# Kernel tuning notes

Measured on AMD Instinct MI355X. Metric: run time of the kernel, lower is better.

Reference implementation:

```python
import jax, jax.numpy as jnp
import numpy as np
import math

L, DIN, DZ, H, C, NQ, NP = 768, 384, 128, 12, 16, 4, 6
C_SQU = 1.0 / math.sqrt(C)            # scalar qk scale
W_C = math.sqrt(2.0 / (9 * NQ))       # point-distance scale


def _w(key, fan_in, fan_out):
    return jax.random.normal(key, (fan_in, fan_out), dtype=jnp.float32) / math.sqrt(fan_in)


def setup_inputs() -> dict:
    key = jax.random.key(0)
    ks = jax.random.split(key, 20)
    inp = {
        "s": jax.random.normal(ks[0], (L, DIN), dtype=jnp.float32),
        "z": jax.random.normal(ks[1], (L, L, DZ), dtype=jnp.float32),
        "rot": jax.random.normal(ks[2], (L, 3, 3), dtype=jnp.float32),
        "trans": jax.random.normal(ks[3], (L, 3), dtype=jnp.float32),
        "Wq1": _w(ks[4], DIN, H * C),
        "Wk1": _w(ks[5], DIN, H * C),
        "Wv1": _w(ks[6], DIN, H * C),
        "Wq2": _w(ks[7], DIN, H * NQ * 3),
        "Wk2": _w(ks[8], DIN, H * NQ * 3),
        "Wv3": _w(ks[9], DIN, H * NP * 3),
        "Wz": _w(ks[10], DZ, H),
        "W1": _w(ks[11], H * DZ, DIN),
        "b1": jnp.zeros((DIN,), dtype=jnp.float32),
        "W2": _w(ks[12], H * C, DIN),
        "b2": jnp.zeros((DIN,), dtype=jnp.float32),
        "W3": _w(ks[13], H * NP * 3, DIN),
        "b3": jnp.zeros((DIN,), dtype=jnp.float32),
        "gamma": jnp.zeros((H,), dtype=jnp.float32),
    }
    return inp


def ipa_transform(x, rot, trans):
    # x: [L,H,P,3] local points -> global: rot @ x + trans
    return jnp.einsum('lij,lhpj->lhpi', rot, x) + trans[:, None, None, :]


def ipa_inverse_transform(x, rot, trans):
    # global -> local: rot^T @ (x - trans)
    return jnp.einsum('lji,lhpj->lhpi', rot, x - trans[:, None, None, :])


def reference(s, z, rot, trans, Wq1, Wk1, Wv1, Wq2, Wk2, Wv3, Wz,
              W1, b1, W2, b2, W3, b3, gamma):
    q1 = (s @ Wq1).reshape(L, H, C)
    k1 = (s @ Wk1).reshape(L, H, C)
    v1 = (s @ Wv1).reshape(L, H, C)
    att = jnp.einsum('ihc,jhc->ijh', q1, k1) * C_SQU          # [L,L,H]
    bias_z = z @ Wz                                           # [L,L,H]
    q2 = ipa_transform((s @ Wq2).reshape(L, H, NQ, 3), rot, trans)
    k2 = ipa_transform((s @ Wk2).reshape(L, H, NQ, 3), rot, trans)
    # squared-distance map sum over query points & xyz, via |q|^2+|k|^2-2qk
    sq = jnp.sum(q2 * q2, axis=(-2, -1))                      # [L,H]
    sk = jnp.sum(k2 * k2, axis=(-2, -1))                      # [L,H]
    cross = jnp.einsum('ihqt,jhqt->ijh', q2, k2)              # [L,L,H]
    dismap = sq[:, None, :] + sk[None, :, :] - 2.0 * cross
    # NOTE: no softmax in the original module — raw scores weight the values.
    att = att + bias_z - jax.nn.softplus(gamma)[None, None, :] * dismap * (W_C * 0.5)
    o1 = jnp.einsum('ijh,ijd->ihd', att, z)                   # [L,H,DZ]
    o2 = jnp.einsum('jhc,ijh->ihc', v1, att)                  # [L,H,C]
    v3 = ipa_transform((s @ Wv3).reshape(L, H, NP, 3), rot, trans)
    o3 = ipa_inverse_transform(jnp.einsum('jhpt,ijh->ihpt', v3, att), rot, trans)
    out = (o1.reshape(L, -1) @ W1 + b1) \
        + (o2.reshape(L, -1) @ W2 + b2) \
        + (o3.reshape(L, -1) @ W3 + b3)
    return out
```

## Files before the change

### kernel.cpp

```cpp
#include <hip/hip_runtime.h>
#include <math.h>
#include <stdint.h>

#define LL 768
#define DIN 384
#define HH 12
#define NLIN 1080
#define WC_HALF 0.11785113019775792f
#define C_SQU 0.25f

#define OFF_LIN    0u
#define OFF_V1P    829440u
#define OFF_V3P    903168u
#define OFF_QBH    986112u
#define OFF_QBL    1133568u
#define OFF_KBH    1281024u
#define OFF_KBL    1428480u
#define OFF_WZ     1575936u
#define OFF_SQWH   1576960u
#define OFF_SKWH   1586176u
#define OFF_SX     1595392u
#define OFF_O1     8673280u
#define OFF_O2     9852928u
#define OFF_O3     10000384u

typedef __attribute__((ext_vector_type(8))) short short8v;
typedef __attribute__((ext_vector_type(4))) float float4v;

__device__ __forceinline__ ushort f2bu(float f) {
    union { float f; uint32_t u; } v; v.f = f;
    uint32_t r = (v.u + 0x7FFFu + ((v.u >> 16) & 1u)) >> 16;
    return (ushort)r;
}
__device__ __forceinline__ float bu2f(ushort u) {
    union { uint32_t u; float f; } v; v.u = ((uint32_t)u) << 16; return v.f;
}
__device__ __forceinline__ float blo2f(uint32_t u) {
    union { uint32_t u; float f; } v; v.u = u << 16; return v.f;
}
__device__ __forceinline__ float bhi2f(uint32_t u) {
    union { uint32_t u; float f; } v; v.u = u & 0xFFFF0000u; return v.f;
}
__device__ __forceinline__ int fswz(int j) {
    return (((j >> 3) << 1) | ((j >> 1) & 1)) << 4;
}

__global__ __launch_bounds__(256) void gemm_lin_kernel(
    const float* __restrict__ s,
    const float* __restrict__ Wq1, const float* __restrict__ Wk1,
    const float* __restrict__ Wv1, const float* __restrict__ Wq2,
    const float* __restrict__ Wk2, const float* __restrict__ Wv3,
    float* __restrict__ lin)
{
    const int n0 = blockIdx.x * 64;
    const int i0 = blockIdx.y * 64;
    const int tid = threadIdx.x;
    __shared__ float sT[64][17];
    __shared__ float wT[16][65];
    const int tc = tid & 15, tr = tid >> 4;
    float acc[4][4] = {};
    for (int k0 = 0; k0 < DIN; k0 += 16) {
        __syncthreads();
        for (int idx = tid; idx < 1024; idx += 256) {
            int r = idx >> 4, kk = idx & 15;
            sT[r][kk] = s[(size_t)(i0 + r) * DIN + k0 + kk];
        }
        for (int idx = tid; idx < 1024; idx += 256) {
            int kk = idx >> 6, c = idx & 63;
            int col = n0 + c;
            float v = 0.f;
            if (col < NLIN) {
                const float* W; int nout, cc2;
                if      (col < 192) { W = Wq1; nout = 192; cc2 = col; }
                else if (col < 384) { W = Wk1; nout = 192; cc2 = col - 192; }
                else if (col < 576) { W = Wv1; nout = 192; cc2 = col - 384; }
                else if (col < 720) { W = Wq2; nout = 144; cc2 = col - 576; }
                else if (col < 864) { W = Wk2; nout = 144; cc2 = col - 720; }
                else                { W = Wv3; nout = 216; cc2 = col - 864; }
                v = W[(size_t)(k0 + kk) * nout + cc2];
            }
            wT[kk][c] = v;
        }
        __syncthreads();
        #pragma unroll
        for (int kk = 0; kk < 16; ++kk) {
            float a[4], b[4];
            #pragma unroll
            for (int r = 0; r < 4; ++r) a[r] = sT[tr * 4 + r][kk];
            #pragma unroll
            for (int c = 0; c < 4; ++c) b[c] = wT[kk][tc * 4 + c];
            #pragma unroll
            for (int r = 0; r < 4; ++r)
                #pragma unroll
                for (int c = 0; c < 4; ++c) acc[r][c] += a[r] * b[c];
        }
    }
    for (int r = 0; r < 4; ++r)
        for (int c = 0; c < 4; ++c) {
            int col = n0 + tc * 4 + c;
            if (col < NLIN)
                lin[(size_t)(i0 + tr * 4 + r) * NLIN + col] = acc[r][c];
        }
}

__global__ __launch_bounds__(192) void transform_kernel(
    const float* __restrict__ lin, const float* __restrict__ rot,
    const float* __restrict__ trans, const float* __restrict__ gamma,
    const float* __restrict__ Wz,
    ushort* __restrict__ v1q, ushort* __restrict__ v3q,
    ushort* __restrict__ qbh, ushort* __restrict__ qbl,
    ushort* __restrict__ kbh, ushort* __restrict__ kbl,
    ushort* __restrict__ wzpack,
    float* __restrict__ sqwh, float* __restrict__ skwh)
{
    const int l = blockIdx.x;
    const int tid = threadIdx.x;
    __shared__ float q2s[144], k2s[144], sqp[48], skp[48];
    __shared__ float v3s[216];
    __shared__ float whs[12];
    __shared__ float R[9], T[3];
    if (tid < 9) R[tid] = rot[l * 9 + tid];
    if (tid >= 9 && tid < 12) T[tid - 9] = trans[l * 3 + tid - 9];
    __syncthreads();
    if (tid < 48) {
        const float* x = &lin[(size_t)l * NLIN + 576 + tid * 3];
        float x0 = x[0], x1 = x[1], x2 = x[2], ss = 0.f;
        #pragma unroll
        for (int i2 = 0; i2 < 3; ++i2) {
            float v = R[i2*3+0]*x0 + R[i2*3+1]*x1 + R[i2*3+2]*x2 + T[i2];
            q2s[tid * 3 + i2] = v; ss += v * v;
        }
        sqp[tid] = ss;
    } else if (tid < 96) {
        int t2 = tid - 48;
        const float* x = &lin[(size_t)l * NLIN + 720 + t2 * 3];
        float x0 = x[0], x1 = x[1], x2 = x[2], ss = 0.f;
        #pragma unroll
        for (int i2 = 0; i2 < 3; ++i2) {
            float v = R[i2*3+0]*x0 + R[i2*3+1]*x1 + R[i2*3+2]*x2 + T[i2];
            k2s[t2 * 3 + i2] = v; ss += v * v;
        }
        skp[t2] = ss;
    } else if (tid < 168) {
        int t2 = tid - 96;
        const float* x = &lin[(size_t)l * NLIN + 864 + t2 * 3];
        float x0 = x[0], x1 = x[1], x2 = x[2];
        #pragma unroll
        for (int i2 = 0; i2 < 3; ++i2) {
            float v = R[i2*3+0]*x0 + R[i2*3+1]*x1 + R[i2*3+2]*x2 + T[i2];
            v3s[t2 * 3 + i2] = v;
        }
    }
    __syncthreads();
    if (tid < 12) {
        float sq = sqp[tid*4] + sqp[tid*4+1] + sqp[tid*4+2] + sqp[tid*4+3];
        float sk = skp[tid*4] + skp[tid*4+1] + skp[tid*4+2] + skp[tid*4+3];
        float w = logf(1.0f + expf(gamma[tid])) * WC_HALF;
        whs[tid] = w;
        sqwh[tid * 768 + l] = w * sq;
        skwh[tid * 768 + l] = w * sk;
    }
    __syncthreads();
    const int tt = l >> 5, jj = l & 31;
    if (tid < 192)
        v1q[((size_t)tt * 192 + tid) * 32 + jj] =
            f2bu(lin[(size_t)l * NLIN + 384 + tid]);
    for (int c = tid; c < 216; c += 192)
        v3q[((size_t)tt * 216 + c) * 32 + jj] = f2bu(v3s[c]);
    for (int idx = tid; idx < 384; idx += 192) {
        int h = idx >> 5, k = idx & 31;
        float qv, kv;
        if (k < 16) {
            qv = lin[(size_t)l * NLIN + h * 16 + k];
            kv = C_SQU * lin[(size_t)l * NLIN + 192 + h * 16 + k];
        } else if (k < 28) {
            int u = k - 16;
            qv = q2s[h * 12 + u];
            kv = 2.0f * whs[h] * k2s[h * 12 + u];
        } else { qv = 0.0f; kv = 0.0f; }
        size_t base = ((size_t)h * 768 + l) * 32 + k;
        ushort qh = f2bu(qv), kh = f2bu(kv);
        qbh[base] = qh; qbl[base] = f2bu(qv - bu2f(qh));
        kbh[base] = kh; kbl[base] = f2bu(kv - bu2f(kh));
    }
    if (l == 0) {
        for (int idx = tid; idx < 2048; idx += 192) {
            int kb = idx >> 9, lane = (idx >> 3) & 63, e = idx & 7;
            int d = kb * 32 + (lane >> 4) * 8 + e, h = lane & 15;
            wzpack[idx] = (h < 12) ? f2bu(Wz[d * 12 + h]) : (ushort)0;
        }
    }
}

__global__ __launch_bounds__(256) void sextra_kernel(
    const ushort* __restrict__ qbh, const ushort* __restrict__ qbl,
    const ushort* __restrict__ kbh, const ushort* __restrict__ kbl,
    const float* __restrict__ sqwh, const float* __restrict__ skwh,
    float* __restrict__ sx)
{
    const int tid = threadIdx.x;
    const int wv = tid >> 6, lane = tid & 63, lm = lane & 15, g = lane >> 4;
    const int i0 = blockIdx.x * 16;
    const int jb = blockIdx.y * 64 + wv * 16;
    #pragma unroll 4
    for (int h = 0; h < 12; ++h) {
        size_t qoff = ((size_t)h * 768 + i0 + lm) * 32 + g * 8;
        size_t koff = ((size_t)h * 768 + jb + lm) * 32 + g * 8;
        short8v ah = *(const short8v*)(qbh + qoff);
        short8v al = *(const short8v*)(qbl + qoff);
        short8v bh = *(const short8v*)(kbh + koff);
        short8v bl = *(const short8v*)(kbl + koff);
        float4v c1 = {0.f, 0.f, 0.f, 0.f};
        float4v c2 = {0.f, 0.f, 0.f, 0.f};
        c1 = __builtin_amdgcn_mfma_f32_16x16x32_bf16(ah, bh, c1, 0, 0, 0);
        c2 = __builtin_amdgcn_mfma_f32_16x16x32_bf16(ah, bl, c2, 0, 0, 0);
        c2 = __builtin_amdgcn_mfma_f32_16x16x32_bf16(al, bh, c2, 0, 0, 0);
        float skv = skwh[h * 768 + jb + lm];
        #pragma unroll
        for (int r = 0; r < 4; ++r) {
            int ii = i0 + g * 4 + r;
            sx[((size_t)ii * 12 + h) * 768 + jb + lm] =
                (c1[r] + c2[r]) - sqwh[h * 768 + ii] - skv;
        }
    }
}

__global__ __launch_bounds__(256) void attn_kernel(
    const float* __restrict__ z, const ushort* __restrict__ v1q,
    const ushort* __restrict__ v3q, const float* __restrict__ sx,
    const ushort* __restrict__ wzp,
    const float* __restrict__ rot, const float* __restrict__ trans,
    float* __restrict__ o1, float* __restrict__ o2, float* __restrict__ o3l)
{
    const int i = blockIdx.x, tid = threadIdx.x;
    const int wv = tid >> 6, lane = tid & 63, lm = lane & 15, g = lane >> 4;
    __shared__ __attribute__((aligned(16))) char zrow[2][32 * 256];
    __shared__ __attribute__((aligned(16))) char attbh[16 * 80];
    __shared__ __attribute__((aligned(16))) char attbl[16 * 80];
    __shared__ __attribute__((aligned(16))) float attf[16][36];
    __shared__ float o3s[216];

    short8v wzf[4];
    #pragma unroll
    for (int kb = 0; kb < 4; ++kb)
        wzf[kb] = *(const short8v*)(wzp + (kb * 64 + lane) * 8);

    const float4* zsrc = (const float4*)(z + (size_t)i * (LL * 128));
    const int jA = wv * 16 + lm;
    const int h2 = tid >> 4;
    const int h3 = tid / 18;

    {
        float4 z0[4];
        #pragma unroll
        for (int s = 0; s < 4; ++s) z0[s] = zsrc[s * 256 + tid];
        #pragma unroll
        for (int s = 0; s < 4; ++s) {
            int k4 = s * 256 + tid, j = k4 >> 5, d0 = (k4 & 31) * 4;
            float4 v = z0[s];
            ushort b0 = f2bu(v.x), b1 = f2bu(v.y), b2 = f2bu(v.z), b3 = f2bu(v.w);
            uint32_t lo = b0 | ((uint32_t)b1 << 16), hi = b2 | ((uint32_t)b3 << 16);
            *(uint64_t*)(&zrow[0][j * 256 + ((d0 * 2) ^ fswz(j))]) =
                (uint64_t)lo | ((uint64_t)hi << 32);
        }
    }
    float sxr[4] = {0.f, 0.f, 0.f, 0.f};
    if (wv < 2 && g < 3) {
        #pragma unroll
        for (int r = 0; r < 4; ++r)
            sxr[r] = sx[((size_t)i * 12 + g * 4 + r) * 768 + jA];
    }
    __syncthreads();

    float4v acc1[2] = {{0.f,0.f,0.f,0.f}, {0.f,0.f,0.f,0.f}};
    float acc2 = 0.f, acc3 = 0.f;
    int p = 0;

    for (int t = 0; t < 24; ++t) {
        const int j0 = t * 32;
        float4 zreg[4];
        if (t < 23) {
            #pragma unroll
            for (int s = 0; s < 4; ++s)
                zreg[s] = zsrc[(size_t)(t + 1) * 1024 + s * 256 + tid];
        }
        uint4 v1x[4], v3x[4];
        if (tid < 192) {
            const uint4* pv = (const uint4*)(v1q + ((size_t)t * 192 + tid) * 32);
            #pragma unroll
            for (int c4 = 0; c4 < 4; ++c4) v1x[c4] = pv[c4];
        }
        if (tid < 216) {
            const uint4* pv = (const uint4*)(v3q + ((size_t)t * 216 + tid) * 32);
            #pragma unroll
            for (int c4 = 0; c4 < 4; ++c4) v3x[c4] = pv[c4];
        }
        float sxn[4] = {0.f, 0.f, 0.f, 0.f};
        if (wv < 2 && g < 3 && t < 23) {
            #pragma unroll
            for (int r = 0; r < 4; ++r)
                sxn[r] = sx[((size_t)i * 12 + g * 4 + r) * 768 + j0 + 32 + jA];
        }
        if (wv < 2) {
            float4v bias = {0.f, 0.f, 0.f, 0.f};
            #pragma unroll
            for (int kb = 0; kb < 4; ++kb) {
                short8v bz = *(const short8v*)(
                    &zrow[p][jA * 256 + ((kb * 64 + g * 16) ^ fswz(jA))]);
                bias = __builtin_amdgcn_mfma_f32_16x16x32_bf16(wzf[kb], bz, bias, 0, 0, 0);
            }
            #pragma unroll
            for (int r = 0; r < 4; ++r) {
                int h = g * 4 + r;
                float att = bias[r] + sxr[r];
                attf[h][jA] = att;
                ushort hi = f2bu(att);
                *(ushort*)(&attbh[h * 80 + jA * 2]) = hi;
                *(ushort*)(&attbl[h * 80 + jA * 2]) = f2bu(att - bu2f(hi));
            }
        }
        __syncthreads();
        {
            short8v ah = *(const short8v*)(&attbh[lm * 80 + g * 16]);
            short8v al = *(const short8v*)(&attbl[lm * 80 + g * 16]);
            #pragma unroll
            for (int q = 0; q < 2; ++q) {
                const int b = wv * 2 + q;
                short8v bf;
                #pragma unroll
                for (int e = 0; e < 8; ++e) {
                    int jj = g * 8 + e;
                    bf[e] = *(const short*)(&zrow[p][jj * 256 +
                              (((b * 16 + lm) * 2) ^ fswz(jj))]);
                }
                acc1[q] = __builtin_amdgcn_mfma_f32_16x16x32_bf16(ah, bf, acc1[q], 0, 0, 0);
                acc1[q] = __builtin_amdgcn_mfma_f32_16x16x32_bf16(al, bf, acc1[q], 0, 0, 0);
            }
        }
        if (tid < 192) {
            const float4* af = (const float4*)(&attf[h2][0]);
            #pragma unroll
            for (int c4 = 0; c4 < 4; ++c4) {
                float4 a0 = af[2 * c4], a1 = af[2 * c4 + 1];
                uint4 w = v1x[c4];
                acc2 += a0.x * blo2f(w.x) + a0.y * bhi2f(w.x)
                      + a0.z * blo2f(w.y) + a0.w * bhi2f(w.y)
                      + a1.x * blo2f(w.z) + a1.y * bhi2f(w.z)
                      + a1.z * blo2f(w.w) + a1.w * bhi2f(w.w);
            }
        }
        if (tid < 216) {
            const float4* af = (const float4*)(&attf[h3][0]);
            #pragma unroll
            for (int c4 = 0; c4 < 4; ++c4) {
                float4 a0 = af[2 * c4], a1 = af[2 * c4 + 1];
                uint4 w = v3x[c4];
                acc3 += a0.x * blo2f(w.x) + a0.y * bhi2f(w.x)
                      + a0.z * blo2f(w.y) + a0.w * bhi2f(w.y)
                      + a1.x * blo2f(w.z) + a1.y * bhi2f(w.z)
                      + a1.z * blo2f(w.w) + a1.w * bhi2f(w.w);
            }
        }
        if (t < 23) {
            #pragma unroll
            for (int s = 0; s < 4; ++s) {
                int k4 = s * 256 + tid, j = k4 >> 5, d0 = (k4 & 31) * 4;
                float4 v = zreg[s];
                ushort b0 = f2bu(v.x), b1 = f2bu(v.y), b2 = f2bu(v.z), b3 = f2bu(v.w);
                uint32_t lo = b0 | ((uint32_t)b1 << 16), hi = b2 | ((uint32_t)b3 << 16);
                *(uint64_t*)(&zrow[p ^ 1][j * 256 + ((d0 * 2) ^ fswz(j))]) =
                    (uint64_t)lo | ((uint64_t)hi << 32);
            }
        }
        __syncthreads();
        #pragma unroll
        for (int r = 0; r < 4; ++r) sxr[r] = sxn[r];
        p ^= 1;
    }
    if (g < 3) {
        #pragma unroll
        for (int q = 0; q < 2; ++q) {
            const int b = wv * 2 + q;
            #pragma unroll
            for (int r = 0; r < 4; ++r)
                o1[(size_t)i * 1536 + (g * 4 + r) * 128 + b * 16 + lm] = acc1[q][r];
        }
    }
    if (tid < 192) o2[(size_t)i * 192 + tid] = acc2;
    if (tid < 216) o3s[tid] = acc3;
    __syncthreads();
    if (tid < 72) {
        float x0 = o3s[tid * 3 + 0] - trans[i * 3 + 0];
        float x1 = o3s[tid * 3 + 1] - trans[i * 3 + 1];
        float x2 = o3s[tid * 3 + 2] - trans[i * 3 + 2];
        const float* R = &rot[(size_t)i * 9];
        o3l[(size_t)i * 216 + tid * 3 + 0] = R[0]*x0 + R[3]*x1 + R[6]*x2;
        o3l[(size_t)i * 216 + tid * 3 + 1] = R[1]*x0 + R[4]*x1 + R[7]*x2;
        o3l[(size_t)i * 216 + tid * 3 + 2] = R[2]*x0 + R[5]*x1 + R[8]*x2;
    }
}

#define KCH 324
__global__ __launch_bounds__(384) void proj_kernel(
    const float* __restrict__ o1, const float* __restrict__ o2,
    const float* __restrict__ o3l,
    const float* __restrict__ W1, const float* __restrict__ W2,
    const float* __restrict__ W3,
    float* __restrict__ part)
{
    const int it = blockIdx.x, kt = blockIdx.y;
    const int tid = threadIdx.x;
    const int kbeg = kt * KCH, kend = kbeg + KCH;
    __shared__ float olds[16][KCH];
    for (int idx = tid; idx < 16 * KCH; idx += 384) {
        int r = idx / KCH, kk = idx % KCH;
        int k = kbeg + kk;
        int i = it * 16 + r;
        float v;
        if (k < 1536)      v = o1[(size_t)i * 1536 + k];
        else if (k < 1728) v = o2[(size_t)i * 192 + k - 1536];
        else               v = o3l[(size_t)i * 216 + k - 1728];
        olds[r][kk] = v;
    }
    __syncthreads();
    float acc[16] = {};
    {
        int s0 = kbeg, s1 = (kend < 1536) ? kend : 1536;
        for (int k = s0; k < s1; ++k) {
            float w = W1[(size_t)k * 384 + tid];
            int kk = k - kbeg;
            #pragma unroll
            for (int r = 0; r < 16; ++r) acc[r] += olds[r][kk] * w;
        }
    }
    {
        int s0 = (kbeg > 1536) ? kbeg : 1536, s1 = (kend < 1728) ? kend : 1728;
        for (int k = s0; k < s1; ++k) {
            float w = W2[(size_t)(k - 1536) * 384 + tid];
            int kk = k - kbeg;
            #pragma unroll
            for (int r = 0; r < 16; ++r) acc[r] += olds[r][kk] * w;
        }
    }
    {
        int s0 = (kbeg > 1728) ? kbeg : 1728, s1 = kend;
        for (int k = s0; k < s1; ++k) {
            float w = W3[(size_t)(k - 1728) * 384 + tid];
            int kk = k - kbeg;
            #pragma unroll
            for (int r = 0; r < 16; ++r) acc[r] += olds[r][kk] * w;
        }
    }
    for (int r = 0; r < 16; ++r)
        part[((size_t)kt * LL + it * 16 + r) * 384 + tid] = acc[r];
}

__global__ __launch_bounds__(256) void final_kernel(
    const float* __restrict__ part,
    const float* __restrict__ b1, const float* __restrict__ b2,
    const float* __restrict__ b3, float* __restrict__ out)
{
    int idx = blockIdx.x * 256 + threadIdx.x;
    if (idx < LL * 384) {
        int n = idx % 384;
        float v = b1[n] + b2[n] + b3[n];
        #pragma unroll
        for (int kt = 0; kt < 6; ++kt) v += part[(size_t)kt * 294912 + idx];
        out[idx] = v;
    }
}

extern "C" void kernel_launch(void* const* d_in, const int* in_sizes, int n_in,
                              void* d_out, int out_size, void* d_ws, size_t ws_size,
                              hipStream_t stream) {
    const float* s     = (const float*)d_in[0];
    const float* z     = (const float*)d_in[1];
    const float* rot   = (const float*)d_in[2];
    const float* trans = (const float*)d_in[3];
    const float* Wq1   = (const float*)d_in[4];
    const float* Wk1   = (const float*)d_in[5];
    const float* Wv1   = (const float*)d_in[6];
    const float* Wq2   = (const float*)d_in[7];
    const float* Wk2   = (const float*)d_in[8];
    const float* Wv3   = (const float*)d_in[9];
    const float* Wz    = (const float*)d_in[10];
    const float* W1    = (const float*)d_in[11];
    const float* b1    = (const float*)d_in[12];
    const float* W2    = (const float*)d_in[13];
    const float* b2    = (const float*)d_in[14];
    const float* W3    = (const float*)d_in[15];
    const float* b3    = (const float*)d_in[16];
    const float* gamma = (const float*)d_in[17];
    float* ws  = (float*)d_ws;
    float* out = (float*)d_out;

    float*  lin  = ws + OFF_LIN;
    ushort* v1q  = (ushort*)(ws + OFF_V1P);
    ushort* v3q  = (ushort*)(ws + OFF_V3P);
    ushort* qbh  = (ushort*)(ws + OFF_QBH);
    ushort* qbl  = (ushort*)(ws + OFF_QBL);
    ushort* kbh  = (ushort*)(ws + OFF_KBH);
    ushort* kbl  = (ushort*)(ws + OFF_KBL);
    ushort* wzp  = (ushort*)(ws + OFF_WZ);
    float*  sqwh = ws + OFF_SQWH;
    float*  skwh = ws + OFF_SKWH;
    float*  sx   = ws + OFF_SX;
    float*  o1   = ws + OFF_O1;
    float*  o2   = ws + OFF_O2;
    float*  o3l  = ws + OFF_O3;
    float*  part = ws + OFF_SX;

    dim3 gA(17, 12);
    gemm_lin_kernel<<<gA, 256, 0, stream>>>(s, Wq1, Wk1, Wv1, Wq2, Wk2, Wv3, lin);
    transform_kernel<<<LL, 192, 0, stream>>>(lin, rot, trans, gamma, Wz,
                                             v1q, v3q, qbh, qbl, kbh, kbl, wzp,
                                             sqwh, skwh);
    dim3 gS(48, 12);
    sextra_kernel<<<gS, 256, 0, stream>>>(qbh, qbl, kbh, kbl, sqwh, skwh, sx);
    attn_kernel<<<LL, 256, 0, stream>>>(z, v1q, v3q, sx, wzp, rot, trans,
                                        o1, o2, o3l);
    dim3 gC(48, 6);
    proj_kernel<<<gC, 384, 0, stream>>>(o1, o2, o3l, W1, W2, W3, part);
    final_kernel<<<(LL * 384 + 255) / 256, 256, 0, stream>>>(part, b1, b2, b3, out);
}
```

Before: 333.2 us.

## Split attention j-range across two blocks per row with separate reduction kernel

Each attention row is now processed by two blocks, each covering half of the key range (12 of 24 tiles). Partial o1/o2/o3 sums go to new workspace buffers, and a new reduce kernel adds them and applies the inverse frame transform. This doubles the grid to 1536 blocks, so the 768-block launch fills the GPU's compute units more evenly. The cost is an extra kernel launch, partial-sum write and read traffic, and a shorter per-block pipeline.

Measured after the change: 325.0 us. 1.03x faster.

```diff
diff --git a/kernel.cpp b/kernel.cpp
--- a/kernel.cpp
+++ b/kernel.cpp
@@ -23,6 +23,9 @@
 #define OFF_O1     8673280u
 #define OFF_O2     9852928u
 #define OFF_O3     10000384u
+#define OFF_PO1    10166272u
+#define OFF_PO2    12525568u
+#define OFF_PO3    12820480u
 
 typedef __attribute__((ext_vector_type(8))) short short8v;
 typedef __attribute__((ext_vector_type(4))) float float4v;
@@ -229,16 +232,16 @@
     const float* __restrict__ z, const ushort* __restrict__ v1q,
     const ushort* __restrict__ v3q, const float* __restrict__ sx,
     const ushort* __restrict__ wzp,
-    const float* __restrict__ rot, const float* __restrict__ trans,
-    float* __restrict__ o1, float* __restrict__ o2, float* __restrict__ o3l)
-{
-    const int i = blockIdx.x, tid = threadIdx.x;
+    float* __restrict__ po1, float* __restrict__ po2, float* __restrict__ po3)
+{
+    const int bid = blockIdx.x, tid = threadIdx.x;
+    const int i = bid >> 1, half = bid & 1;
+    const int t0 = half * 12;
     const int wv = tid >> 6, lane = tid & 63, lm = lane & 15, g = lane >> 4;
     __shared__ __attribute__((aligned(16))) char zrow[2][32 * 256];
     __shared__ __attribute__((aligned(16))) char attbh[16 * 80];
     __shared__ __attribute__((aligned(16))) char attbl[16 * 80];
     __shared__ __attribute__((aligned(16))) float attf[16][36];
-    __shared__ float o3s[216];
 
     short8v wzf[4];
     #pragma unroll
@@ -253,7 +256,7 @@
     {
         float4 z0[4];
         #pragma unroll
-        for (int s = 0; s < 4; ++s) z0[s] = zsrc[s * 256 + tid];
+        for (int s = 0; s < 4; ++s) z0[s] = zsrc[(size_t)t0 * 1024 + s * 256 + tid];
         #pragma unroll
         for (int s = 0; s < 4; ++s) {
             int k4 = s * 256 + tid, j = k4 >> 5, d0 = (k4 & 31) * 4;
@@ -268,7 +271,7 @@
     if (wv < 2 && g < 3) {
         #pragma unroll
         for (int r = 0; r < 4; ++r)
-            sxr[r] = sx[((size_t)i * 12 + g * 4 + r) * 768 + jA];
+            sxr[r] = sx[((size_t)i * 12 + g * 4 + r) * 768 + t0 * 32 + jA];
     }
     __syncthreads();
 
@@ -276,27 +279,28 @@
     float acc2 = 0.f, acc3 = 0.f;
     int p = 0;
 
-    for (int t = 0; t < 24; ++t) {
-        const int j0 = t * 32;
+    for (int t = 0; t < 12; ++t) {
+        const int tt = t0 + t;
+        const int j0 = tt * 32;
         float4 zreg[4];
-        if (t < 23) {
+        if (t < 11) {
             #pragma unroll
             for (int s = 0; s < 4; ++s)
-                zreg[s] = zsrc[(size_t)(t + 1) * 1024 + s * 256 + tid];
+                zreg[s] = zsrc[(size_t)(tt + 1) * 1024 + s * 256 + tid];
         }
         uint4 v1x[4], v3x[4];
         if (tid < 192) {
-            const uint4* pv = (const uint4*)(v1q + ((size_t)t * 192 + tid) * 32);
+            const uint4* pv = (const uint4*)(v1q + ((size_t)tt * 192 + tid) * 32);
             #pragma unroll
             for (int c4 = 0; c4 < 4; ++c4) v1x[c4] = pv[c4];
         }
         if (tid < 216) {
-            const uint4* pv = (const uint4*)(v3q + ((size_t)t * 216 + tid) * 32);
+            const uint4* pv = (const uint4*)(v3q + ((size_t)tt * 216 + tid) * 32);
             #pragma unroll
             for (int c4 = 0; c4 < 4; ++c4) v3x[c4] = pv[c4];
         }
         float sxn[4] = {0.f, 0.f, 0.f, 0.f};
-        if (wv < 2 && g < 3 && t < 23) {
+        if (wv < 2 && g < 3 && t < 11) {
             #pragma unroll
             for (int r = 0; r < 4; ++r)
                 sxn[r] = sx[((size_t)i * 12 + g * 4 + r) * 768 + j0 + 32 + jA];
@@ -361,7 +365,7 @@
                       + a1.z * blo2f(w.w) + a1.w * bhi2f(w.w);
             }
         }
-        if (t < 23) {
+        if (t < 11) {
             #pragma unroll
             for (int s = 0; s < 4; ++s) {
                 int k4 = s * 256 + tid, j = k4 >> 5, d0 = (k4 & 31) * 4;
@@ -383,11 +387,30 @@
             const int b = wv * 2 + q;
             #pragma unroll
             for (int r = 0; r < 4; ++r)
-                o1[(size_t)i * 1536 + (g * 4 + r) * 128 + b * 16 + lm] = acc1[q][r];
-        }
-    }
-    if (tid < 192) o2[(size_t)i * 192 + tid] = acc2;
-    if (tid < 216) o3s[tid] = acc3;
+                po1[(size_t)bid * 1536 + (g * 4 + r) * 128 + b * 16 + lm] = acc1[q][r];
+        }
+    }
+    if (tid < 192) po2[(size_t)bid * 192 + tid] = acc2;
+    if (tid < 216) po3[(size_t)bid * 216 + tid] = acc3;
+}
+
+__global__ __launch_bounds__(256) void reduce_kernel(
+    const float* __restrict__ po1, const float* __restrict__ po2,
+    const float* __restrict__ po3,
+    const float* __restrict__ rot, const float* __restrict__ trans,
+    float* __restrict__ o1, float* __restrict__ o2, float* __restrict__ o3l)
+{
+    const int i = blockIdx.x, tid = threadIdx.x;
+    __shared__ float o3s[216];
+    const size_t a1 = (size_t)(2 * i) * 1536, b1 = (size_t)(2 * i + 1) * 1536;
+    for (int c = tid; c < 1536; c += 256)
+        o1[(size_t)i * 1536 + c] = po1[a1 + c] + po1[b1 + c];
+    if (tid < 192)
+        o2[(size_t)i * 192 + tid] = po2[(size_t)(2 * i) * 192 + tid]
+                                  + po2[(size_t)(2 * i + 1) * 192 + tid];
+    if (tid < 216)
+        o3s[tid] = po3[(size_t)(2 * i) * 216 + tid]
+                 + po3[(size_t)(2 * i + 1) * 216 + tid];
     __syncthreads();
     if (tid < 72) {
         float x0 = o3s[tid * 3 + 0] - trans[i * 3 + 0];
@@ -508,6 +531,9 @@
     float*  o1   = ws + OFF_O1;
     float*  o2   = ws + OFF_O2;
     float*  o3l  = ws + OFF_O3;
+    float*  po1  = ws + OFF_PO1;
+    float*  po2  = ws + OFF_PO2;
+    float*  po3  = ws + OFF_PO3;
     float*  part = ws + OFF_SX;
 
     dim3 gA(17, 12);
@@ -517,8 +543,8 @@
                                              sqwh, skwh);
     dim3 gS(48, 12);
     sextra_kernel<<<gS, 256, 0, stream>>>(qbh, qbl, kbh, kbl, sqwh, skwh, sx);
-    attn_kernel<<<LL, 256, 0, stream>>>(z, v1q, v3q, sx, wzp, rot, trans,
-                                        o1, o2, o3l);
+    attn_kernel<<<LL * 2, 256, 0, stream>>>(z, v1q, v3q, sx, wzp, po1, po2, po3);
+    reduce_kernel<<<LL, 256, 0, stream>>>(po1, po2, po3, rot, trans, o1, o2, o3l);
     dim3 gC(48, 6);
     proj_kernel<<<gC, 384, 0, stream>>>(o1, o2, o3l, W1, W2, W3, part);
     final_kernel<<<(LL * 384 + 255) / 256, 256, 0, stream>>>(part, b1, b2, b3, out);
```

## Split attention over j-halves, move value products to MFMA kernel, fuse final reduction

Applied to the files above, without the earlier changes.

The attention kernel now splits each row's j range across two blocks and only computes the z-weighted output, writing full attention scores back into the sx buffer. A new ov_kernel computes the v1 and v3 weighted sums per head with bf16 hi/lo MFMAs over a transposed value layout, then applies the inverse frame transform. sextra gets one block per head, and the projection kernel loops over all K chunks itself, summing the two partial o1 halves and adding biases so the final reduction kernel goes away. This trades scalar per-thread value dot products and the attention kernel's serial j loop for more parallelism and tensor-core use, at the cost of an extra read and write of the attention matrix and fewer blocks in the projection.

Result: slower. 702.6 us (+110.9%).

```diff
diff --git a/kernel.cpp b/kernel.cpp
--- a/kernel.cpp
+++ b/kernel.cpp
@@ -10,19 +10,18 @@
 #define C_SQU 0.25f
 
 #define OFF_LIN    0u
-#define OFF_V1P    829440u
-#define OFF_V3P    903168u
-#define OFF_QBH    986112u
-#define OFF_QBL    1133568u
-#define OFF_KBH    1281024u
-#define OFF_KBL    1428480u
-#define OFF_WZ     1575936u
-#define OFF_SQWH   1576960u
-#define OFF_SKWH   1586176u
-#define OFF_SX     1595392u
-#define OFF_O1     8673280u
-#define OFF_O2     9852928u
-#define OFF_O3     10000384u
+#define OFF_VT     829440u
+#define OFF_QBH    1050624u
+#define OFF_QBL    1198080u
+#define OFF_KBH    1345536u
+#define OFF_KBL    1492992u
+#define OFF_WZ     1640448u
+#define OFF_SQWH   1641472u
+#define OFF_SKWH   1650688u
+#define OFF_SX     1659904u
+#define OFF_O2     8737792u
+#define OFF_O3     8885248u
+#define OFF_PO1    9051136u
 
 typedef __attribute__((ext_vector_type(8))) short short8v;
 typedef __attribute__((ext_vector_type(4))) float float4v;
@@ -34,12 +33,6 @@
 }
 __device__ __forceinline__ float bu2f(ushort u) {
     union { uint32_t u; float f; } v; v.u = ((uint32_t)u) << 16; return v.f;
-}
-__device__ __forceinline__ float blo2f(uint32_t u) {
-    union { uint32_t u; float f; } v; v.u = u << 16; return v.f;
-}
-__device__ __forceinline__ float bhi2f(uint32_t u) {
-    union { uint32_t u; float f; } v; v.u = u & 0xFFFF0000u; return v.f;
 }
 __device__ __forceinline__ int fswz(int j) {
     return (((j >> 3) << 1) | ((j >> 1) & 1)) << 4;
@@ -107,7 +100,7 @@
     const float* __restrict__ lin, const float* __restrict__ rot,
     const float* __restrict__ trans, const float* __restrict__ gamma,
     const float* __restrict__ Wz,
-    ushort* __restrict__ v1q, ushort* __restrict__ v3q,
+    ushort* __restrict__ vT,
     ushort* __restrict__ qbh, ushort* __restrict__ qbl,
     ushort* __restrict__ kbh, ushort* __restrict__ kbl,
     ushort* __restrict__ wzpack,
@@ -161,12 +154,12 @@
         skwh[tid * 768 + l] = w * sk;
     }
     __syncthreads();
-    const int tt = l >> 5, jj = l & 31;
-    if (tid < 192)
-        v1q[((size_t)tt * 192 + tid) * 32 + jj] =
-            f2bu(lin[(size_t)l * NLIN + 384 + tid]);
-    for (int c = tid; c < 216; c += 192)
-        v3q[((size_t)tt * 216 + c) * 32 + jj] = f2bu(v3s[c]);
+    for (int w = tid; w < 408; w += 192) {
+        int h = w / 34, c = w % 34;
+        float v = (c < 16) ? lin[(size_t)l * NLIN + 384 + h * 16 + c]
+                           : v3s[h * 18 + (c - 16)];
+        vT[((size_t)h * 48 + c) * 768 + l] = f2bu(v);
+    }
     for (int idx = tid; idx < 384; idx += 192) {
         int h = idx >> 5, k = idx & 31;
         float qv, kv;
@@ -202,43 +195,38 @@
     const int wv = tid >> 6, lane = tid & 63, lm = lane & 15, g = lane >> 4;
     const int i0 = blockIdx.x * 16;
     const int jb = blockIdx.y * 64 + wv * 16;
-    #pragma unroll 4
-    for (int h = 0; h < 12; ++h) {
-        size_t qoff = ((size_t)h * 768 + i0 + lm) * 32 + g * 8;
-        size_t koff = ((size_t)h * 768 + jb + lm) * 32 + g * 8;
-        short8v ah = *(const short8v*)(qbh + qoff);
-        short8v al = *(const short8v*)(qbl + qoff);
-        short8v bh = *(const short8v*)(kbh + koff);
-        short8v bl = *(const short8v*)(kbl + koff);
-        float4v c1 = {0.f, 0.f, 0.f, 0.f};
-        float4v c2 = {0.f, 0.f, 0.f, 0.f};
-        c1 = __builtin_amdgcn_mfma_f32_16x16x32_bf16(ah, bh, c1, 0, 0, 0);
-        c2 = __builtin_amdgcn_mfma_f32_16x16x32_bf16(ah, bl, c2, 0, 0, 0);
-        c2 = __builtin_amdgcn_mfma_f32_16x16x32_bf16(al, bh, c2, 0, 0, 0);
-        float skv = skwh[h * 768 + jb + lm];
-        #pragma unroll
-        for (int r = 0; r < 4; ++r) {
-            int ii = i0 + g * 4 + r;
-            sx[((size_t)ii * 12 + h) * 768 + jb + lm] =
-                (c1[r] + c2[r]) - sqwh[h * 768 + ii] - skv;
-        }
+    const int h = blockIdx.z;
+    size_t qoff = ((size_t)h * 768 + i0 + lm) * 32 + g * 8;
+    size_t koff = ((size_t)h * 768 + jb + lm) * 32 + g * 8;
+    short8v ah = *(const short8v*)(qbh + qoff);
+    short8v al = *(const short8v*)(qbl + qoff);
+    short8v bh = *(const short8v*)(kbh + koff);
+    short8v bl = *(const short8v*)(kbl + koff);
+    float4v c1 = {0.f, 0.f, 0.f, 0.f};
+    float4v c2 = {0.f, 0.f, 0.f, 0.f};
+    c1 = __builtin_amdgcn_mfma_f32_16x16x32_bf16(ah, bh, c1, 0, 0, 0);
+    c2 = __builtin_amdgcn_mfma_f32_16x16x32_bf16(ah, bl, c2, 0, 0, 0);
+    c2 = __builtin_amdgcn_mfma_f32_16x16x32_bf16(al, bh, c2, 0, 0, 0);
+    float skv = skwh[h * 768 + jb + lm];
+    #pragma unroll
+    for (int r = 0; r < 4; ++r) {
+        int ii = i0 + g * 4 + r;
+        sx[((size_t)ii * 12 + h) * 768 + jb + lm] =
+            (c1[r] + c2[r]) - sqwh[h * 768 + ii] - skv;
     }
 }
 
 __global__ __launch_bounds__(256) void attn_kernel(
-    const float* __restrict__ z, const ushort* __restrict__ v1q,
-    const ushort* __restrict__ v3q, const float* __restrict__ sx,
-    const ushort* __restrict__ wzp,
-    const float* __restrict__ rot, const float* __restrict__ trans,
-    float* __restrict__ o1, float* __restrict__ o2, float* __restrict__ o3l)
+    const float* __restrict__ z, const ushort* __restrict__ wzp,
+    float* sxa,
+    float* __restrict__ po1)
 {
-    const int i = blockIdx.x, tid = threadIdx.x;
+    const int bid = blockIdx.x, tid = threadIdx.x;
+    const int i = bid >> 1, t0 = (bid & 1) * 12;
     const int wv = tid >> 6, lane = tid & 63, lm = lane & 15, g = lane >> 4;
     __shared__ __attribute__((aligned(16))) char zrow[2][32 * 256];
     __shared__ __attribute__((aligned(16))) char attbh[16 * 80];
     __shared__ __attribute__((aligned(16))) char attbl[16 * 80];
-    __shared__ __attribute__((aligned(16))) float attf[16][36];
-    __shared__ float o3s[216];
 
     short8v wzf[4];
     #pragma unroll
@@ -247,13 +235,11 @@
 
     const float4* zsrc = (const float4*)(z + (size_t)i * (LL * 128));
     const int jA = wv * 16 + lm;
-    const int h2 = tid >> 4;
-    const int h3 = tid / 18;
 
     {
         float4 z0[4];
         #pragma unroll
-        for (int s = 0; s < 4; ++s) z0[s] = zsrc[s * 256 + tid];
+        for (int s = 0; s < 4; ++s) z0[s] = zsrc[(size_t)t0 * 1024 + s * 256 + tid];
         #pragma unroll
         for (int s = 0; s < 4; ++s) {
             int k4 = s * 256 + tid, j = k4 >> 5, d0 = (k4 & 31) * 4;
@@ -268,38 +254,26 @@
     if (wv < 2 && g < 3) {
         #pragma unroll
         for (int r = 0; r < 4; ++r)
-            sxr[r] = sx[((size_t)i * 12 + g * 4 + r) * 768 + jA];
+            sxr[r] = sxa[((size_t)i * 12 + g * 4 + r) * 768 + t0 * 32 + jA];
     }
     __syncthreads();
 
     float4v acc1[2] = {{0.f,0.f,0.f,0.f}, {0.f,0.f,0.f,0.f}};
-    float acc2 = 0.f, acc3 = 0.f;
     int p = 0;
 
-    for (int t = 0; t < 24; ++t) {
-        const int j0 = t * 32;
+    for (int t = 0; t < 12; ++t) {
+        const int tt = t0 + t, j0 = tt * 32;
         float4 zreg[4];
-        if (t < 23) {
+        if (t < 11) {
             #pragma unroll
             for (int s = 0; s < 4; ++s)
-                zreg[s] = zsrc[(size_t)(t + 1) * 1024 + s * 256 + tid];
-        }
-        uint4 v1x[4], v3x[4];
-        if (tid < 192) {
-            const uint4* pv = (const uint4*)(v1q + ((size_t)t * 192 + tid) * 32);
-            #pragma unroll
-            for (int c4 = 0; c4 < 4; ++c4) v1x[c4] = pv[c4];
-        }
-        if (tid < 216) {
-            const uint4* pv = (const uint4*)(v3q + ((size_t)t * 216 + tid) * 32);
-            #pragma unroll
-            for (int c4 = 0; c4 < 4; ++c4) v3x[c4] = pv[c4];
+                zreg[s] = zsrc[(size_t)(tt + 1) * 1024 + s * 256 + tid];
         }
         float sxn[4] = {0.f, 0.f, 0.f, 0.f};
-        if (wv < 2 && g < 3 && t < 23) {
+        if (wv < 2 && g < 3 && t < 11) {
             #pragma unroll
             for (int r = 0; r < 4; ++r)
-                sxn[r] = sx[((size_t)i * 12 + g * 4 + r) * 768 + j0 + 32 + jA];
+                sxn[r] = sxa[((size_t)i * 12 + g * 4 + r) * 768 + j0 + 32 + jA];
         }
         if (wv < 2) {
             float4v bias = {0.f, 0.f, 0.f, 0.f};
@@ -313,10 +287,11 @@
             for (int r = 0; r < 4; ++r) {
                 int h = g * 4 + r;
                 float att = bias[r] + sxr[r];
-                attf[h][jA] = att;
                 ushort hi = f2bu(att);
                 *(ushort*)(&attbh[h * 80 + jA * 2]) = hi;
                 *(ushort*)(&attbl[h * 80 + jA * 2]) = f2bu(att - bu2f(hi));
+                if (g < 3)
+                    sxa[((size_t)i * 12 + h) * 768 + j0 + jA] = att;
             }
         }
         __syncthreads();
@@ -337,31 +312,7 @@
                 acc1[q] = __builtin_amdgcn_mfma_f32_16x16x32_bf16(al, bf, acc1[q], 0, 0, 0);
             }
         }
-        if (tid < 192) {
-            const float4* af = (const float4*)(&attf[h2][0]);
-            #pragma unroll
-            for (int c4 = 0; c4 < 4; ++c4) {
-                float4 a0 = af[2 * c4], a1 = af[2 * c4 + 1];
-                uint4 w = v1x[c4];
-                acc2 += a0.x * blo2f(w.x) + a0.y * bhi2f(w.x)
-                      + a0.z * blo2f(w.y) + a0.w * bhi2f(w.y)
-                      + a1.x * blo2f(w.z) + a1.y * bhi2f(w.z)
-                      + a1.z * blo2f(w.w) + a1.w * bhi2f(w.w);
-            }
-        }
-        if (tid < 216) {
-            const float4* af = (const float4*)(&attf[h3][0]);
-            #pragma unroll
-            for (int c4 = 0; c4 < 4; ++c4) {
-                float4 a0 = af[2 * c4], a1 = af[2 * c4 + 1];
-                uint4 w = v3x[c4];
-                acc3 += a0.x * blo2f(w.x) + a0.y * bhi2f(w.x)
-                      + a0.z * blo2f(w.y) + a0.w * bhi2f(w.y)
-                      + a1.x * blo2f(w.z) + a1.y * bhi2f(w.z)
-                      + a1.z * blo2f(w.w) + a1.w * bhi2f(w.w);
-            }
-        }
-        if (t < 23) {
+        if (t < 11) {
             #pragma unroll
             for (int s = 0; s < 4; ++s) {
                 int k4 = s * 256 + tid, j = k4 >> 5, d0 = (k4 & 31) * 4;
@@ -383,91 +334,133 @@
             const int b = wv * 2 + q;
             #pragma unroll
             for (int r = 0; r < 4; ++r)
-                o1[(size_t)i * 1536 + (g * 4 + r) * 128 + b * 16 + lm] = acc1[q][r];
-        }
-    }
-    if (tid < 192) o2[(size_t)i * 192 + tid] = acc2;
-    if (tid < 216) o3s[tid] = acc3;
+                po1[(size_t)bid * 1536 + (g * 4 + r) * 128 + b * 16 + lm] = acc1[q][r];
+        }
+    }
+}
+
+__global__ __launch_bounds__(64) void ov_kernel(
+    const float* __restrict__ att, const ushort* __restrict__ vT,
+    const float* __restrict__ rot, const float* __restrict__ trans,
+    float* __restrict__ o2, float* __restrict__ o3l)
+{
+    const int i0 = blockIdx.x * 16;
+    const int h = blockIdx.y;
+    const int lane = threadIdx.x;
+    const int lm = lane & 15, g = lane >> 4;
+    __shared__ float o3s[16][18];
+
+    float4v acc0 = {0.f,0.f,0.f,0.f};
+    float4v acc1 = {0.f,0.f,0.f,0.f};
+    float4v acc2 = {0.f,0.f,0.f,0.f};
+    const float* arow = att + ((size_t)(i0 + lm) * 12 + h) * 768;
+    const ushort* vbase = vT + (size_t)h * 48 * 768;
+    for (int kt = 0; kt < 24; ++kt) {
+        const float4* ap = (const float4*)(arow + kt * 32 + g * 8);
+        float4 a0 = ap[0], a1 = ap[1];
+        float av[8] = {a0.x, a0.y, a0.z, a0.w, a1.x, a1.y, a1.z, a1.w};
+        short8v ah, al;
+        #pragma unroll
+        for (int e = 0; e < 8; ++e) {
+            ushort hi = f2bu(av[e]);
+            ah[e] = (short)hi;
+            al[e] = (short)f2bu(av[e] - bu2f(hi));
+        }
+        const int kq = kt * 32 + g * 8;
+        short8v b0 = *(const short8v*)(vbase + (size_t)(0 * 16 + lm) * 768 + kq);
+        short8v b1 = *(const short8v*)(vbase + (size_t)(1 * 16 + lm) * 768 + kq);
+        short8v b2 = *(const short8v*)(vbase + (size_t)(2 * 16 + lm) * 768 + kq);
+        acc0 = __builtin_amdgcn_mfma_f32_16x16x32_bf16(ah, b0, acc0, 0, 0, 0);
+        acc0 = __builtin_amdgcn_mfma_f32_16x16x32_bf16(al, b0, acc0, 0, 0, 0);
+        acc1 = __builtin_amdgcn_mfma_f32_16x16x32_bf16(ah, b1, acc1, 0, 0, 0);
+        acc1 = __builtin_amdgcn_mfma_f32_16x16x32_bf16(al, b1, acc1, 0, 0, 0);
+        acc2 = __builtin_amdgcn_mfma_f32_16x16x32_bf16(ah, b2, acc2, 0, 0, 0);
+        acc2 = __builtin_amdgcn_mfma_f32_16x16x32_bf16(al, b2, acc2, 0, 0, 0);
+    }
+    #pragma unroll
+    for (int r = 0; r < 4; ++r)
+        o2[(size_t)(i0 + g * 4 + r) * 192 + h * 16 + lm] = acc0[r];
+    #pragma unroll
+    for (int r = 0; r < 4; ++r) {
+        int row = g * 4 + r;
+        o3s[row][lm < 16 ? lm : 0] = acc1[r];
+        if (lm < 2) o3s[row][16 + lm] = acc2[r];
+    }
     __syncthreads();
-    if (tid < 72) {
-        float x0 = o3s[tid * 3 + 0] - trans[i * 3 + 0];
-        float x1 = o3s[tid * 3 + 1] - trans[i * 3 + 1];
-        float x2 = o3s[tid * 3 + 2] - trans[i * 3 + 2];
-        const float* R = &rot[(size_t)i * 9];
-        o3l[(size_t)i * 216 + tid * 3 + 0] = R[0]*x0 + R[3]*x1 + R[6]*x2;
-        o3l[(size_t)i * 216 + tid * 3 + 1] = R[1]*x0 + R[4]*x1 + R[7]*x2;
-        o3l[(size_t)i * 216 + tid * 3 + 2] = R[2]*x0 + R[5]*x1 + R[8]*x2;
+    for (int it = lane; it < 96; it += 64) {
+        int row = it / 6, pp = it % 6;
+        int ii = i0 + row;
+        const float* R = &rot[(size_t)ii * 9];
+        float x0 = o3s[row][pp * 3 + 0] - trans[ii * 3 + 0];
+        float x1 = o3s[row][pp * 3 + 1] - trans[ii * 3 + 1];
+        float x2 = o3s[row][pp * 3 + 2] - trans[ii * 3 + 2];
+        o3l[(size_t)ii * 216 + h * 18 + pp * 3 + 0] = R[0]*x0 + R[3]*x1 + R[6]*x2;
+        o3l[(size_t)ii * 216 + h * 18 + pp * 3 + 1] = R[1]*x0 + R[4]*x1 + R[7]*x2;
+        o3l[(size_t)ii * 216 + h * 18 + pp * 3 + 2] = R[2]*x0 + R[5]*x1 + R[8]*x2;
     }
 }
 
 #define KCH 324
 __global__ __launch_bounds__(384) void proj_kernel(
-    const float* __restrict__ o1, const float* __restrict__ o2,
+    const float* __restrict__ po1, const float* __restrict__ o2,
     const float* __restrict__ o3l,
     const float* __restrict__ W1, const float* __restrict__ W2,
     const float* __restrict__ W3,
-    float* __restrict__ part)
-{
-    const int it = blockIdx.x, kt = blockIdx.y;
-    const int tid = threadIdx.x;
-    const int kbeg = kt * KCH, kend = kbeg + KCH;
-    __shared__ float olds[16][KCH];
-    for (int idx = tid; idx < 16 * KCH; idx += 384) {
-        int r = idx / KCH, kk = idx % KCH;
-        int k = kbeg + kk;
-        int i = it * 16 + r;
-        float v;
-        if (k < 1536)      v = o1[(size_t)i * 1536 + k];
-        else if (k < 1728) v = o2[(size_t)i * 192 + k - 1536];
-        else               v = o3l[(size_t)i * 216 + k - 1728];
-        olds[r][kk] = v;
-    }
-    __syncthreads();
-    float acc[16] = {};
-    {
-        int s0 = kbeg, s1 = (kend < 1536) ? kend : 1536;
-        for (int k = s0; k < s1; ++k) {
-            float w = W1[(size_t)k * 384 + tid];
-            int kk = k - kbeg;
-            #pragma unroll
-            for (int r = 0; r < 16; ++r) acc[r] += olds[r][kk] * w;
-        }
-    }
-    {
-        int s0 = (kbeg > 1536) ? kbeg : 1536, s1 = (kend < 1728) ? kend : 1728;
-        for (int k = s0; k < s1; ++k) {
-            float w = W2[(size_t)(k - 1536) * 384 + tid];
-            int kk = k - kbeg;
-            #pragma unroll
-            for (int r = 0; r < 16; ++r) acc[r] += olds[r][kk] * w;
-        }
-    }
-    {
-        int s0 = (kbeg > 1728) ? kbeg : 1728, s1 = kend;
-        for (int k = s0; k < s1; ++k) {
-            float w = W3[(size_t)(k - 1728) * 384 + tid];
-            int kk = k - kbeg;
-            #pragma unroll
-            for (int r = 0; r < 16; ++r) acc[r] += olds[r][kk] * w;
-        }
-    }
-    for (int r = 0; r < 16; ++r)
-        part[((size_t)kt * LL + it * 16 + r) * 384 + tid] = acc[r];
-}
-
-__global__ __launch_bounds__(256) void final_kernel(
-    const float* __restrict__ part,
     const float* __restrict__ b1, const float* __restrict__ b2,
     const float* __restrict__ b3, float* __restrict__ out)
 {
-    int idx = blockIdx.x * 256 + threadIdx.x;
-    if (idx < LL * 384) {
-        int n = idx % 384;
-        float v = b1[n] + b2[n] + b3[n];
-        #pragma unroll
-        for (int kt = 0; kt < 6; ++kt) v += part[(size_t)kt * 294912 + idx];
-        out[idx] = v;
-    }
+    const int it = blockIdx.x;
+    const int tid = threadIdx.x;
+    __shared__ float olds[16][KCH];
+    float acc[16] = {};
+    for (int kt = 0; kt < 6; ++kt) {
+        const int kbeg = kt * KCH, kend = kbeg + KCH;
+        __syncthreads();
+        for (int idx = tid; idx < 16 * KCH; idx += 384) {
+            int r = idx / KCH, kk = idx % KCH;
+            int k = kbeg + kk;
+            int i = it * 16 + r;
+            float v;
+            if (k < 1536)
+                v = po1[(size_t)(2 * i) * 1536 + k] + po1[(size_t)(2 * i + 1) * 1536 + k];
+            else if (k < 1728)
+                v = o2[(size_t)i * 192 + k - 1536];
+            else
+                v = o3l[(size_t)i * 216 + k - 1728];
+            olds[r][kk] = v;
+        }
+        __syncthreads();
+        {
+            int s0 = kbeg, s1 = (kend < 1536) ? kend : 1536;
+            for (int k = s0; k < s1; ++k) {
+                float w = W1[(size_t)k * 384 + tid];
+                int kk = k - kbeg;
+                #pragma unroll
+                for (int r = 0; r < 16; ++r) acc[r] += olds[r][kk] * w;
+            }
+        }
+        {
+            int s0 = (kbeg > 1536) ? kbeg : 1536, s1 = (kend < 1728) ? kend : 1728;
+            for (int k = s0; k < s1; ++k) {
+                float w = W2[(size_t)(k - 1536) * 384 + tid];
+                int kk = k - kbeg;
+                #pragma unroll
+                for (int r = 0; r < 16; ++r) acc[r] += olds[r][kk] * w;
+            }
+        }
+        {
+            int s0 = (kbeg > 1728) ? kbeg : 1728, s1 = kend;
+            for (int k = s0; k < s1; ++k) {
+                float w = W3[(size_t)(k - 1728) * 384 + tid];
+                int kk = k - kbeg;
+                #pragma unroll
+                for (int r = 0; r < 16; ++r) acc[r] += olds[r][kk] * w;
+            }
+        }
+    }
+    float bb = b1[tid] + b2[tid] + b3[tid];
+    for (int r = 0; r < 16; ++r)
+        out[(size_t)(it * 16 + r) * 384 + tid] = acc[r] + bb;
 }
 
 extern "C" void kernel_launch(void* const* d_in, const int* in_sizes, int n_in,
@@ -495,8 +488,7 @@
     float* out = (float*)d_out;
 
     float*  lin  = ws + OFF_LIN;
-    ushort* v1q  = (ushort*)(ws + OFF_V1P);
-    ushort* v3q  = (ushort*)(ws + OFF_V3P);
+    ushort* vT   = (ushort*)(ws + OFF_VT);
     ushort* qbh  = (ushort*)(ws + OFF_QBH);
     ushort* qbl  = (ushort*)(ws + OFF_QBL);
     ushort* kbh  = (ushort*)(ws + OFF_KBH);
@@ -505,21 +497,20 @@
     float*  sqwh = ws + OFF_SQWH;
     float*  skwh = ws + OFF_SKWH;
     float*  sx   = ws + OFF_SX;
-    float*  o1   = ws + OFF_O1;
     float*  o2   = ws + OFF_O2;
     float*  o3l  = ws + OFF_O3;
-    float*  part = ws + OFF_SX;
+    float*  po1  = ws + OFF_PO1;
 
     dim3 gA(17, 12);
     gemm_lin_kernel<<<gA, 256, 0, stream>>>(s, Wq1, Wk1, Wv1, Wq2, Wk2, Wv3, lin);
     transform_kernel<<<LL, 192, 0, stream>>>(lin, rot, trans, gamma, Wz,
-                                             v1q, v3q, qbh, qbl, kbh, kbl, wzp,
+                                             vT, qbh, qbl, kbh, kbl, wzp,
                                              sqwh, skwh);
-    dim3 gS(48, 12);
+    dim3 gS(48, 12, 12);
     sextra_kernel<<<gS, 256, 0, stream>>>(qbh, qbl, kbh, kbl, sqwh, skwh, sx);
-    attn_kernel<<<LL, 256, 0, stream>>>(z, v1q, v3q, sx, wzp, rot, trans,
-                                        o1, o2, o3l);
-    dim3 gC(48, 6);
-    proj_kernel<<<gC, 384, 0, stream>>>(o1, o2, o3l, W1, W2, W3, part);
-    final_kernel<<<(LL * 384 + 255) / 256, 256, 0, stream>>>(part, b1, b2, b3, out);
-}
+    attn_kernel<<<LL * 2, 256, 0, stream>>>(z, wzp, sx, po1);
+    dim3 gV(48, 12);
+    ov_kernel<<<gV, 64, 0, stream>>>(sx, vT, rot, trans, o2, o3l);
+    proj_kernel<<<48, 384, 0, stream>>>(po1, o2, o3l, W1, W2, W3,
+                                        b1, b2, b3, out);
+}
```
